# Performance work log

Measured on AMD Instinct MI355X. Metric: run time of the kernel, lower is better.

The kernel has to match this reference:

```python
import jax, jax.numpy as jnp
import numpy as np

B, S = 32, 256          # sequences, tokens per sequence (prefill)
DIM, NH, NKV, HD = 2048, 16, 16, 128
CLS, GRID, BASE = 1, 16, 10000


def precompute_freqs_cis_2d(grid_size, n_elem, base, cls_token_num):
    half = n_elem // 2
    freqs = 1.0 / (base ** (np.arange(0, half, 2)[: half // 2].astype(np.float32) / half))
    t = np.arange(grid_size, dtype=np.float32)
    fr = np.outer(t, freqs)                      # [grid, half//2]
    fg = np.concatenate([
        np.broadcast_to(fr[:, None, :], (grid_size, grid_size, fr.shape[1])),
        np.broadcast_to(fr[None, :, :], (grid_size, grid_size, fr.shape[1])),
    ], axis=-1)                                  # [grid, grid, half]
    cache = np.stack([np.cos(fg), np.sin(fg)], axis=-1).reshape(grid_size * grid_size, half, 2)
    cond = np.concatenate([np.zeros((cls_token_num, half, 2), np.float32), cache.astype(np.float32)], axis=0)
    return jnp.asarray(cond)                     # [cls+grid^2, half, 2]

FREQS = precompute_freqs_cis_2d(GRID, HD, BASE, CLS)


def _apply_rope(x, fc):
    # x: [T, H, HD], fc: [T, HD//2, 2]
    xr = x.reshape(x.shape[0], x.shape[1], HD // 2, 2)
    c = fc[:, None, :, 0]
    s = fc[:, None, :, 1]
    out = jnp.stack([xr[..., 0] * c - xr[..., 1] * s,
                     xr[..., 1] * c + xr[..., 0] * s], axis=-1)
    return out.reshape(x.shape)


def setup_inputs() -> dict:
    key = jax.random.key(0)
    k1, k2, k3 = jax.random.split(key, 3)
    x = jax.random.normal(k1, (B * S, DIM), dtype=jnp.float32)
    positions = jnp.tile(jnp.arange(S, dtype=jnp.int32), B)  # per-seq positions 0..S-1
    total_kv = (NH + 2 * NKV) * HD
    wqkv = jax.random.normal(k2, (total_kv, DIM), dtype=jnp.float32) * 0.02
    wo = jax.random.normal(k3, (DIM, DIM), dtype=jnp.float32) * 0.02
    return {"x": x, "positions": positions, "wqkv": wqkv, "wo": wo}


def reference(x, positions, wqkv, wo):
    T = x.shape[0]
    kv_size = NKV * HD
    qkv = x @ wqkv.T                               # [T, dim + 2*kv_size]
    xq, xk, xv = jnp.split(qkv, [DIM, DIM + kv_size], axis=-1)
    q = xq.reshape(T, NH, HD)
    k = xk.reshape(T, NKV, HD)
    v = xv.reshape(T, NKV, HD)

    fc = FREQS[positions]                          # [T, HD//2, 2]
    q = _apply_rope(q, fc)
    k = _apply_rope(k, fc)

    # paged attention (prefill): causal attention within each sequence
    qb = q.reshape(B, S, NH, HD)
    kb = k.reshape(B, S, NKV, HD)
    vb = v.reshape(B, S, NKV, HD)
    scale = HD ** -0.5
    scores = jnp.einsum("bqhd,bkhd->bhqk", qb, kb) * scale   # [B,H,S,S]
    causal = jnp.tril(jnp.ones((S, S), dtype=bool))
    scores = jnp.where(causal[None, None], scores, jnp.finfo(scores.dtype).min)
    attn = jax.nn.softmax(scores, axis=-1)
    out = jnp.einsum("bhqk,bkhd->bqhd", attn, vb).reshape(T, DIM)
    return out @ wo.T
```

## Files before the change

### kernel.cpp

```cpp
#include <hip/hip_runtime.h>
#include <cstddef>


typedef float    f32x4 __attribute__((ext_vector_type(4)));
typedef _Float16 f16x8 __attribute__((ext_vector_type(8)));
typedef _Float16 f16x4 __attribute__((ext_vector_type(4)));

#define LOG2E 1.4426950408889634f
#define NLOG2B_32 (-0.41524101186192697f)

__device__ static inline f32x4 mfma16x32(f16x8 a, f16x8 b, f32x4 c) {
  return __builtin_amdgcn_mfma_f32_16x16x32_f16(a, b, c, 0, 0, 0);
}

__device__ static inline void gload16(const void* g, void* lds) {
  __builtin_amdgcn_global_load_lds(
      (const __attribute__((address_space(1))) unsigned int*)g,
      (__attribute__((address_space(3))) unsigned int*)lds, 16, 0, 0);
}

#define BAR()    asm volatile("s_barrier" ::: "memory")
#define VMCNT6() asm volatile("s_waitcnt vmcnt(6)" ::: "memory")

__global__ void cvt3_f32_f16(const float* __restrict__ s0, _Float16* __restrict__ d0,
                             const float* __restrict__ s1, _Float16* __restrict__ d1,
                             const float* __restrict__ s2, _Float16* __restrict__ d2) {
  int i = blockIdx.x * blockDim.x + threadIdx.x;
  const float* src; _Float16* dst;
  if (i < 4194304)      { src = s0; dst = d0; }
  else if (i < 7340032) { src = s1; dst = d1; i -= 4194304; }
  else                  { src = s2; dst = d2; i -= 7340032; }
  f32x4 v = *(const f32x4*)(src + (size_t)i * 4);
  f16x4 o;
  o[0] = (_Float16)v[0]; o[1] = (_Float16)v[1];
  o[2] = (_Float16)v[2]; o[3] = (_Float16)v[3];
  *(f16x4*)(dst + (size_t)i * 4) = o;
}

template <typename OutT>
__global__ void __launch_bounds__(512, 2)
gemm_bt5(const _Float16* __restrict__ A, const _Float16* __restrict__ Bt,
         OutT* __restrict__ C, int M, int N, int K) {
  __shared__ __attribute__((aligned(16))) _Float16 Ab[2][256 * 64];
  __shared__ __attribute__((aligned(16))) _Float16 Bb[2][256 * 64];

  const int tid  = threadIdx.x;
  const int lane = tid & 63;
  const int w    = tid >> 6;
  const int wm   = w >> 2, wn = w & 3;
  const int g    = lane >> 4, li = lane & 15;

  const int nwg = (int)gridDim.x;
  const int cpx = nwg >> 3;
  const int bid = (int)blockIdx.x;
  const int swz = (bid & 7) * cpx + (bid >> 3);
  const int nbn = N >> 8;
  const int bm  = (swz / nbn) << 8;
  const int bn  = (swz % nbn) << 8;
  const int NT  = K >> 6;

  const int srow = tid >> 3;
  const int scol = ((tid & 7) ^ (srow & 7)) * 8;
  const _Float16* gA = A  + (size_t)(bm + srow) * K + scol;
  const _Float16* gB = Bt + (size_t)(bn + srow) * K + scol;
  const int sdst = w * 1024;

  auto stage = [&](const _Float16* gbase, _Float16* lbase, int h, int kt) {
    const _Float16* gp = gbase + (size_t)h * 128 * K + kt;
    char* lp = (char*)lbase + h * 16384;
#pragma unroll
    for (int j = 0; j < 2; ++j)
      gload16(gp + (size_t)j * 64 * K, lp + j * 8192 + sdst);
  };

  auto rdfrag = [&](const _Float16* buf, int row, int k2) -> f16x8 {
    const int pc = ((k2 << 2) + g) ^ (li & 7);
    return *(const f16x8*)((const char*)buf + row * 128 + pc * 16);
  };

  f32x4 acc[8][4] = {};

  stage(gA, Ab[0], 0, 0);
  stage(gB, Bb[0], 0, 0);
  stage(gB, Bb[0], 1, 0);
  stage(gA, Ab[0], 1, 0);
  stage(gA, Ab[1], 0, (NT > 1) ? 64 : 0);
  VMCNT6();
  BAR();

  for (int T = 0; T < NT; ++T) {
    const int cb = T & 1, nb = cb ^ 1;
    const _Float16* Ac = Ab[cb];
    const _Float16* Bc = Bb[cb];
    const int ktN  = (T + 1 < NT) ? (T + 1) << 6 : 0;
    const int ktN2 = (T + 2 < NT) ? (T + 2) << 6 : 0;

    f16x8 af0[4][2], af1[4][2], bf0[2][2], bf1[2][2];

#pragma unroll
    for (int m = 0; m < 4; ++m)
#pragma unroll
      for (int k2 = 0; k2 < 2; ++k2)
        af0[m][k2] = rdfrag(Ac, wm * 128 + m * 16 + li, k2);
#pragma unroll
    for (int n = 0; n < 2; ++n)
#pragma unroll
      for (int k2 = 0; k2 < 2; ++k2)
        bf0[n][k2] = rdfrag(Bc, wn * 64 + n * 16 + li, k2);
    stage(gB, Bb[nb], 0, ktN);
    __builtin_amdgcn_s_setprio(1);
#pragma unroll
    for (int m = 0; m < 4; ++m)
#pragma unroll
      for (int n = 0; n < 2; ++n)
#pragma unroll
        for (int k2 = 0; k2 < 2; ++k2)
          acc[m][n] = mfma16x32(af0[m][k2], bf0[n][k2], acc[m][n]);
    __builtin_amdgcn_s_setprio(0);
    VMCNT6();
    BAR();

#pragma unroll
    for (int n = 0; n < 2; ++n)
#pragma unroll
      for (int k2 = 0; k2 < 2; ++k2)
        bf1[n][k2] = rdfrag(Bc, wn * 64 + (n + 2) * 16 + li, k2);
    stage(gB, Bb[nb], 1, ktN);
    __builtin_amdgcn_s_setprio(1);
#pragma unroll
    for (int m = 0; m < 4; ++m)
#pragma unroll
      for (int n = 0; n < 2; ++n)
#pragma unroll
        for (int k2 = 0; k2 < 2; ++k2)
          acc[m][n + 2] = mfma16x32(af0[m][k2], bf1[n][k2], acc[m][n + 2]);
    __builtin_amdgcn_s_setprio(0);
    VMCNT6();
    BAR();

#pragma unroll
    for (int m = 0; m < 4; ++m)
#pragma unroll
      for (int k2 = 0; k2 < 2; ++k2)
        af1[m][k2] = rdfrag(Ac, wm * 128 + (m + 4) * 16 + li, k2);
    stage(gA, Ab[nb], 1, ktN);
    __builtin_amdgcn_s_setprio(1);
#pragma unroll
    for (int m = 0; m < 4; ++m)
#pragma unroll
      for (int n = 0; n < 2; ++n)
#pragma unroll
        for (int k2 = 0; k2 < 2; ++k2)
          acc[m + 4][n] = mfma16x32(af1[m][k2], bf0[n][k2], acc[m + 4][n]);
    __builtin_amdgcn_s_setprio(0);
    VMCNT6();
    BAR();

    stage(gA, Ab[cb], 0, ktN2);
    __builtin_amdgcn_s_setprio(1);
#pragma unroll
    for (int m = 0; m < 4; ++m)
#pragma unroll
      for (int n = 0; n < 2; ++n)
#pragma unroll
        for (int k2 = 0; k2 < 2; ++k2)
          acc[m + 4][n + 2] = mfma16x32(af1[m][k2], bf1[n][k2], acc[m + 4][n + 2]);
    __builtin_amdgcn_s_setprio(0);
    VMCNT6();
    BAR();
  }

  asm volatile("s_waitcnt vmcnt(0)" ::: "memory");

#pragma unroll
  for (int m = 0; m < 8; ++m)
#pragma unroll
    for (int n = 0; n < 4; ++n)
#pragma unroll
      for (int r = 0; r < 4; ++r) {
        const int row = bm + wm * 128 + m * 16 + g * 4 + r;
        const int col = bn + wn * 64 + n * 16 + li;
        C[(size_t)row * N + col] = (OutT)acc[m][n][r];
      }
}

__global__ void rope_kernel(_Float16* __restrict__ qkv,
                            const int* __restrict__ positions) {
  const int idx = blockIdx.x * blockDim.x + threadIdx.x;
  const int ch = idx & 15;
  const int hh = (idx >> 4) & 31;
  const int t  = idx >> 9;
  _Float16* p = qkv + (size_t)t * 6144 + hh * 128 + ch * 8;
  const int pos = positions[t];
  f16x8 v = *(const f16x8*)p;
  f16x8 o;
  if (pos == 0) {
#pragma unroll
    for (int u = 0; u < 8; ++u) o[u] = (_Float16)0.f;
  } else {
    const int gi = pos - 1;
    const float tv = (ch < 8) ? (float)(gi >> 4) : (float)(gi & 15);
#pragma unroll
    for (int u = 0; u < 4; ++u) {
      const int k2 = (ch * 4 + u) & 31;
      const float freq = exp2f((float)k2 * NLOG2B_32);
      const float ang = tv * freq;
      float s, c;
      sincosf(ang, &s, &c);
      const float x0 = (float)v[2 * u];
      const float x1 = (float)v[2 * u + 1];
      o[2 * u]     = (_Float16)(x0 * c - x1 * s);
      o[2 * u + 1] = (_Float16)(x1 * c + x0 * s);
    }
  }
  *(f16x8*)p = o;
}

__global__ void __launch_bounds__(512)
attn_kernel(const _Float16* __restrict__ qkv, _Float16* __restrict__ O) {
  const int b  = blockIdx.x >> 4;
  const int h  = blockIdx.x & 15;
  const int tb = b << 8;
  const int tid = threadIdx.x;
  const int lane = tid & 63;
  const int w = tid >> 6;
  const int g = lane >> 4, li = lane & 15;

  __shared__ __attribute__((aligned(16))) _Float16 Ks[64 * 128];
  __shared__ __attribute__((aligned(16))) _Float16 Vt[128 * 64];
  __shared__ __attribute__((aligned(16))) _Float16 Ps[8][32 * 40];

  const int qb[2]   = {w, 15 - w};
  const int qrow[2] = {qb[0] * 16, qb[1] * 16};
  const int kmax[2] = {qb[0] >> 2, qb[1] >> 2};

  f16x8 qf[2][4];
#pragma unroll
  for (int rb = 0; rb < 2; ++rb)
#pragma unroll
    for (int ks = 0; ks < 4; ++ks)
      qf[rb][ks] = *(const f16x8*)(qkv + (size_t)(tb + qrow[rb] + li) * 6144
                                   + h * 128 + ks * 32 + g * 8);

  f32x4 oacc[2][8] = {};
  float m_r[2][4], l_r[2][4];
#pragma unroll
  for (int rb = 0; rb < 2; ++rb)
#pragma unroll
    for (int r = 0; r < 4; ++r) { m_r[rb][r] = -1e30f; l_r[rb][r] = 0.f; }

  const float scale = 0.08838834764831845f;

  for (int kt = 0; kt < 4; ++kt) {
#pragma unroll
    for (int i = 0; i < 2; ++i) {
      const int s = i * 512 + tid;
      const int key = s >> 4;
      const int sch = (s & 15) ^ (key & 7);
      const _Float16* gk = qkv + (size_t)(tb + kt * 64 + key) * 6144
                           + 2048 + h * 128 + sch * 8;
      gload16(gk, (char*)Ks + (i * 512 + (tid & ~63)) * 16);
    }
#pragma unroll
    for (int i = 0; i < 2; ++i) {
      const int s = i * 512 + tid;
      const int key = s >> 4;
      const int chv = s & 15;
      f16x8 v = *(const f16x8*)(qkv + (size_t)(tb + kt * 64 + key) * 6144
                                + 4096 + h * 128 + chv * 8);
#pragma unroll
      for (int e = 0; e < 8; ++e) {
        const int d = chv * 8 + e;
        const int blk = ((key >> 3) ^ (d & 7) ^ ((d >> 3) & 7)) & 7;
        Vt[d * 64 + blk * 8 + (key & 7)] = v[e];
      }
    }
    __syncthreads();

    const bool act[2] = {kt <= kmax[0], kt <= kmax[1]};
    if (act[0] || act[1]) {
      f32x4 sacc[2][4] = {};
#pragma unroll
      for (int ks = 0; ks < 4; ++ks) {
        f16x8 kf[4];
#pragma unroll
        for (int cb = 0; cb < 4; ++cb) {
          const int key = cb * 16 + li;
          const int chunk = (ks * 4 + g) ^ (key & 7);
          kf[cb] = *(const f16x8*)((const char*)Ks + key * 256 + chunk * 16);
        }
#pragma unroll
        for (int rb = 0; rb < 2; ++rb)
          if (act[rb])
#pragma unroll
            for (int cb = 0; cb < 4; ++cb)
              sacc[rb][cb] = mfma16x32(qf[rb][ks], kf[cb], sacc[rb][cb]);
      }
#pragma unroll
      for (int rb = 0; rb < 2; ++rb) {
        if (!act[rb]) continue;
#pragma unroll
        for (int r = 0; r < 4; ++r) {
          const int q = qrow[rb] + g * 4 + r;
          float mx = -1e30f;
#pragma unroll
          for (int cb = 0; cb < 4; ++cb) {
            float sv = sacc[rb][cb][r] * scale;
            const int key = kt * 64 + cb * 16 + li;
            sv = (key <= q) ? sv : -1e30f;
            sacc[rb][cb][r] = sv;
            mx = fmaxf(mx, sv);
          }
#pragma unroll
          for (int off = 1; off < 16; off <<= 1)
            mx = fmaxf(mx, __shfl_xor(mx, off));
          const float mold = m_r[rb][r];
          const float mnew = fmaxf(mold, mx);
          const float alpha = exp2f((mold - mnew) * LOG2E);
          float rsum = 0.f;
#pragma unroll
          for (int cb = 0; cb < 4; ++cb) {
            const float pv = exp2f((sacc[rb][cb][r] - mnew) * LOG2E);
            sacc[rb][cb][r] = pv;
            rsum += pv;
          }
#pragma unroll
          for (int off = 1; off < 16; off <<= 1)
            rsum += __shfl_xor(rsum, off);
          m_r[rb][r] = mnew;
          l_r[rb][r] = l_r[rb][r] * alpha + rsum;
#pragma unroll
          for (int db = 0; db < 8; ++db)
            oacc[rb][db][r] *= alpha;
        }
      }
#pragma unroll
      for (int ks2 = 0; ks2 < 2; ++ks2) {
#pragma unroll
        for (int rb = 0; rb < 2; ++rb) {
          if (!act[rb]) continue;
#pragma unroll
          for (int cbh = 0; cbh < 2; ++cbh) {
            const int cb = ks2 * 2 + cbh;
#pragma unroll
            for (int r = 0; r < 4; ++r)
              Ps[w][(rb * 16 + g * 4 + r) * 40 + cbh * 16 + li] =
                  (_Float16)sacc[rb][cb][r];
          }
        }
        asm volatile("s_waitcnt lgkmcnt(0)" ::: "memory");
        f16x8 pa[2];
#pragma unroll
        for (int rb = 0; rb < 2; ++rb)
          if (act[rb])
            pa[rb] = *(const f16x8*)(&Ps[w][(rb * 16 + li) * 40 + g * 8]);
#pragma unroll
        for (int db = 0; db < 8; ++db) {
          const int d = db * 16 + li;
          const int keych = ks2 * 4 + g;
          const int blk = (keych ^ (d & 7) ^ ((d >> 3) & 7)) & 7;
          const f16x8 vf = *(const f16x8*)(&Vt[d * 64 + blk * 8]);
#pragma unroll
          for (int rb = 0; rb < 2; ++rb)
            if (act[rb])
              oacc[rb][db] = mfma16x32(pa[rb], vf, oacc[rb][db]);
        }
      }
    }
    __syncthreads();
  }
#pragma unroll
  for (int rb = 0; rb < 2; ++rb)
#pragma unroll
    for (int db = 0; db < 8; ++db)
#pragma unroll
      for (int r = 0; r < 4; ++r) {
        const int row = tb + qrow[rb] + g * 4 + r;
        const int col = h * 128 + db * 16 + li;
        O[(size_t)row * 2048 + col] = (_Float16)(oacc[rb][db][r] / l_r[rb][r]);
      }
}

extern "C" void kernel_launch(void* const* d_in, const int* in_sizes, int n_in,
                              void* d_out, int out_size, void* d_ws, size_t ws_size,
                              hipStream_t stream) {
  const float* x         = (const float*)d_in[0];
  const int*   positions = (const int*)d_in[1];
  const float* wqkv      = (const float*)d_in[2];
  const float* wo        = (const float*)d_in[3];
  float* out = (float*)d_out;

  char* ws = (char*)d_ws;
  _Float16* qkv    = (_Float16*)(ws);
  _Float16* xf     = (_Float16*)(ws + 100663296);
  _Float16* wqkvf  = (_Float16*)(ws + 134217728);
  _Float16* wof    = (_Float16*)(ws + 159383552);
  _Float16* of     = xf;

  cvt3_f32_f16<<<32768, 256, 0, stream>>>(x, xf, wqkv, wqkvf, wo, wof);

  gemm_bt5<_Float16><<<768, 512, 0, stream>>>(xf, wqkvf, qkv, 8192, 6144, 2048);

  rope_kernel<<<16384, 256, 0, stream>>>(qkv, positions);

  attn_kernel<<<512, 512, 0, stream>>>(qkv, of);

  gemm_bt5<float><<<256, 512, 0, stream>>>(of, wof, out, 8192, 2048, 2048);
}
```

Before: 367.8 us.

## Fuse RoPE into attention and restructure GEMM staging into K-halves

```diff
diff --git a/kernel.cpp b/kernel.cpp
--- a/kernel.cpp
+++ b/kernel.cpp
@@ -20,7 +20,7 @@
 }
 
 #define BAR()    asm volatile("s_barrier" ::: "memory")
-#define VMCNT6() asm volatile("s_waitcnt vmcnt(6)" ::: "memory")
+#define VMCNT4() asm volatile("s_waitcnt vmcnt(4)" ::: "memory")
 
 __global__ void cvt3_f32_f16(const float* __restrict__ s0, _Float16* __restrict__ d0,
                              const float* __restrict__ s1, _Float16* __restrict__ d1,
@@ -39,7 +39,7 @@
 
 template <typename OutT>
 __global__ void __launch_bounds__(512, 2)
-gemm_bt5(const _Float16* __restrict__ A, const _Float16* __restrict__ Bt,
+gemm_bt7(const _Float16* __restrict__ A, const _Float16* __restrict__ Bt,
          OutT* __restrict__ C, int M, int N, int K) {
   __shared__ __attribute__((aligned(16))) _Float16 Ab[2][256 * 64];
   __shared__ __attribute__((aligned(16))) _Float16 Bb[2][256 * 64];
@@ -59,114 +59,100 @@
   const int bn  = (swz % nbn) << 8;
   const int NT  = K >> 6;
 
-  const int srow = tid >> 3;
-  const int scol = ((tid & 7) ^ (srow & 7)) * 8;
+  const int srow = tid >> 2;
+  const int scol = ((tid & 3) ^ ((tid >> 3) & 3)) * 8;
   const _Float16* gA = A  + (size_t)(bm + srow) * K + scol;
   const _Float16* gB = Bt + (size_t)(bn + srow) * K + scol;
   const int sdst = w * 1024;
 
-  auto stage = [&](const _Float16* gbase, _Float16* lbase, int h, int kt) {
-    const _Float16* gp = gbase + (size_t)h * 128 * K + kt;
-    char* lp = (char*)lbase + h * 16384;
+  auto stage = [&](const _Float16* gbase, _Float16* lbase, int kh, int kt) {
+    const _Float16* gp = gbase + kh * 32 + kt;
+    char* lp = (char*)lbase + kh * 16384;
 #pragma unroll
     for (int j = 0; j < 2; ++j)
-      gload16(gp + (size_t)j * 64 * K, lp + j * 8192 + sdst);
+      gload16(gp + (size_t)j * 128 * K, lp + j * 8192 + sdst);
   };
 
-  auto rdfrag = [&](const _Float16* buf, int row, int k2) -> f16x8 {
-    const int pc = ((k2 << 2) + g) ^ (li & 7);
-    return *(const f16x8*)((const char*)buf + row * 128 + pc * 16);
+  auto rdfrag = [&](const _Float16* buf, int row, int kh) -> f16x8 {
+    const int pc = g ^ ((row >> 1) & 3);
+    return *(const f16x8*)((const char*)buf + kh * 16384 + row * 64 + pc * 16);
   };
 
   f32x4 acc[8][4] = {};
 
   stage(gA, Ab[0], 0, 0);
   stage(gB, Bb[0], 0, 0);
+  stage(gA, Ab[0], 1, 0);
   stage(gB, Bb[0], 1, 0);
-  stage(gA, Ab[0], 1, 0);
-  stage(gA, Ab[1], 0, (NT > 1) ? 64 : 0);
-  VMCNT6();
+  asm volatile("s_waitcnt vmcnt(0)" ::: "memory");
   BAR();
 
   for (int T = 0; T < NT; ++T) {
     const int cb = T & 1, nb = cb ^ 1;
     const _Float16* Ac = Ab[cb];
     const _Float16* Bc = Bb[cb];
-    const int ktN  = (T + 1 < NT) ? (T + 1) << 6 : 0;
-    const int ktN2 = (T + 2 < NT) ? (T + 2) << 6 : 0;
-
-    f16x8 af0[4][2], af1[4][2], bf0[2][2], bf1[2][2];
-
-#pragma unroll
-    for (int m = 0; m < 4; ++m)
-#pragma unroll
-      for (int k2 = 0; k2 < 2; ++k2)
-        af0[m][k2] = rdfrag(Ac, wm * 128 + m * 16 + li, k2);
+    const int ktN = (T + 1 < NT) ? (T + 1) << 6 : 0;
+
+    f16x8 af[8], bf[2], bf2[2];
+
+#pragma unroll
+    for (int m = 0; m < 8; ++m)
+      af[m] = rdfrag(Ac, wm * 128 + m * 16 + li, 0);
 #pragma unroll
     for (int n = 0; n < 2; ++n)
-#pragma unroll
-      for (int k2 = 0; k2 < 2; ++k2)
-        bf0[n][k2] = rdfrag(Bc, wn * 64 + n * 16 + li, k2);
+      bf[n] = rdfrag(Bc, wn * 64 + n * 16 + li, 0);
+    stage(gA, Ab[nb], 0, ktN);
+    __builtin_amdgcn_s_setprio(1);
+#pragma unroll
+    for (int m = 0; m < 8; ++m)
+#pragma unroll
+      for (int n = 0; n < 2; ++n)
+        acc[m][n] = mfma16x32(af[m], bf[n], acc[m][n]);
+    __builtin_amdgcn_s_setprio(0);
+    BAR();
+
+#pragma unroll
+    for (int n = 0; n < 2; ++n)
+      bf2[n] = rdfrag(Bc, wn * 64 + (n + 2) * 16 + li, 0);
     stage(gB, Bb[nb], 0, ktN);
     __builtin_amdgcn_s_setprio(1);
 #pragma unroll
-    for (int m = 0; m < 4; ++m)
+    for (int m = 0; m < 8; ++m)
 #pragma unroll
       for (int n = 0; n < 2; ++n)
-#pragma unroll
-        for (int k2 = 0; k2 < 2; ++k2)
-          acc[m][n] = mfma16x32(af0[m][k2], bf0[n][k2], acc[m][n]);
+        acc[m][n + 2] = mfma16x32(af[m], bf2[n], acc[m][n + 2]);
     __builtin_amdgcn_s_setprio(0);
-    VMCNT6();
+    VMCNT4();
     BAR();
 
 #pragma unroll
+    for (int m = 0; m < 8; ++m)
+      af[m] = rdfrag(Ac, wm * 128 + m * 16 + li, 1);
+#pragma unroll
     for (int n = 0; n < 2; ++n)
-#pragma unroll
-      for (int k2 = 0; k2 < 2; ++k2)
-        bf1[n][k2] = rdfrag(Bc, wn * 64 + (n + 2) * 16 + li, k2);
+      bf[n] = rdfrag(Bc, wn * 64 + n * 16 + li, 1);
+    stage(gA, Ab[nb], 1, ktN);
+    __builtin_amdgcn_s_setprio(1);
+#pragma unroll
+    for (int m = 0; m < 8; ++m)
+#pragma unroll
+      for (int n = 0; n < 2; ++n)
+        acc[m][n] = mfma16x32(af[m], bf[n], acc[m][n]);
+    __builtin_amdgcn_s_setprio(0);
+    BAR();
+
+#pragma unroll
+    for (int n = 0; n < 2; ++n)
+      bf2[n] = rdfrag(Bc, wn * 64 + (n + 2) * 16 + li, 1);
     stage(gB, Bb[nb], 1, ktN);
     __builtin_amdgcn_s_setprio(1);
 #pragma unroll
-    for (int m = 0; m < 4; ++m)
+    for (int m = 0; m < 8; ++m)
 #pragma unroll
       for (int n = 0; n < 2; ++n)
-#pragma unroll
-        for (int k2 = 0; k2 < 2; ++k2)
-          acc[m][n + 2] = mfma16x32(af0[m][k2], bf1[n][k2], acc[m][n + 2]);
+        acc[m][n + 2] = mfma16x32(af[m], bf2[n], acc[m][n + 2]);
     __builtin_amdgcn_s_setprio(0);
-    VMCNT6();
-    BAR();
-
-#pragma unroll
-    for (int m = 0; m < 4; ++m)
-#pragma unroll
-      for (int k2 = 0; k2 < 2; ++k2)
-        af1[m][k2] = rdfrag(Ac, wm * 128 + (m + 4) * 16 + li, k2);
-    stage(gA, Ab[nb], 1, ktN);
-    __builtin_amdgcn_s_setprio(1);
-#pragma unroll
-    for (int m = 0; m < 4; ++m)
-#pragma unroll
-      for (int n = 0; n < 2; ++n)
-#pragma unroll
-        for (int k2 = 0; k2 < 2; ++k2)
-          acc[m + 4][n] = mfma16x32(af1[m][k2], bf0[n][k2], acc[m + 4][n]);
-    __builtin_amdgcn_s_setprio(0);
-    VMCNT6();
-    BAR();
-
-    stage(gA, Ab[cb], 0, ktN2);
-    __builtin_amdgcn_s_setprio(1);
-#pragma unroll
-    for (int m = 0; m < 4; ++m)
-#pragma unroll
-      for (int n = 0; n < 2; ++n)
-#pragma unroll
-        for (int k2 = 0; k2 < 2; ++k2)
-          acc[m + 4][n + 2] = mfma16x32(af1[m][k2], bf1[n][k2], acc[m + 4][n + 2]);
-    __builtin_amdgcn_s_setprio(0);
-    VMCNT6();
+    VMCNT4();
     BAR();
   }
 
@@ -184,40 +170,9 @@
       }
 }
 
-__global__ void rope_kernel(_Float16* __restrict__ qkv,
-                            const int* __restrict__ positions) {
-  const int idx = blockIdx.x * blockDim.x + threadIdx.x;
-  const int ch = idx & 15;
-  const int hh = (idx >> 4) & 31;
-  const int t  = idx >> 9;
-  _Float16* p = qkv + (size_t)t * 6144 + hh * 128 + ch * 8;
-  const int pos = positions[t];
-  f16x8 v = *(const f16x8*)p;
-  f16x8 o;
-  if (pos == 0) {
-#pragma unroll
-    for (int u = 0; u < 8; ++u) o[u] = (_Float16)0.f;
-  } else {
-    const int gi = pos - 1;
-    const float tv = (ch < 8) ? (float)(gi >> 4) : (float)(gi & 15);
-#pragma unroll
-    for (int u = 0; u < 4; ++u) {
-      const int k2 = (ch * 4 + u) & 31;
-      const float freq = exp2f((float)k2 * NLOG2B_32);
-      const float ang = tv * freq;
-      float s, c;
-      sincosf(ang, &s, &c);
-      const float x0 = (float)v[2 * u];
-      const float x1 = (float)v[2 * u + 1];
-      o[2 * u]     = (_Float16)(x0 * c - x1 * s);
-      o[2 * u + 1] = (_Float16)(x1 * c + x0 * s);
-    }
-  }
-  *(f16x8*)p = o;
-}
-
 __global__ void __launch_bounds__(512)
-attn_kernel(const _Float16* __restrict__ qkv, _Float16* __restrict__ O) {
+attn_kernel(const _Float16* __restrict__ qkv, _Float16* __restrict__ O,
+            const int* __restrict__ positions) {
   const int b  = blockIdx.x >> 4;
   const int h  = blockIdx.x & 15;
   const int tb = b << 8;
@@ -229,6 +184,17 @@
   __shared__ __attribute__((aligned(16))) _Float16 Ks[64 * 128];
   __shared__ __attribute__((aligned(16))) _Float16 Vt[128 * 64];
   __shared__ __attribute__((aligned(16))) _Float16 Ps[8][32 * 40];
+  __shared__ float2 tab[512];
+  __shared__ int    ptab[256];
+
+  {
+    const float ang = (float)(tid >> 5) * exp2f((float)(tid & 31) * NLOG2B_32);
+    float s, c;
+    sincosf(ang, &s, &c);
+    tab[tid] = make_float2(c, s);
+    if (tid < 256) ptab[tid] = positions[tb + tid];
+  }
+  __syncthreads();
 
   const int qb[2]   = {w, 15 - w};
   const int qrow[2] = {qb[0] * 16, qb[1] * 16};
@@ -236,11 +202,30 @@
 
   f16x8 qf[2][4];
 #pragma unroll
-  for (int rb = 0; rb < 2; ++rb)
-#pragma unroll
-    for (int ks = 0; ks < 4; ++ks)
-      qf[rb][ks] = *(const f16x8*)(qkv + (size_t)(tb + qrow[rb] + li) * 6144
-                                   + h * 128 + ks * 32 + g * 8);
+  for (int rb = 0; rb < 2; ++rb) {
+    const int pos = ptab[qrow[rb] + li];
+    const int iv = (pos - 1) >> 4, jv = (pos - 1) & 15;
+#pragma unroll
+    for (int ks = 0; ks < 4; ++ks) {
+      f16x8 v = *(const f16x8*)(qkv + (size_t)(tb + qrow[rb] + li) * 6144
+                                + h * 128 + ks * 32 + g * 8);
+      f16x8 o;
+      if (pos == 0) {
+#pragma unroll
+        for (int u = 0; u < 8; ++u) o[u] = (_Float16)0.f;
+      } else {
+        const int tv = (ks < 2) ? iv : jv;
+#pragma unroll
+        for (int u = 0; u < 4; ++u) {
+          const float2 cs = tab[tv * 32 + ((ks * 16 + g * 4 + u) & 31)];
+          const float x0 = (float)v[2 * u], x1 = (float)v[2 * u + 1];
+          o[2 * u]     = (_Float16)(x0 * cs.x - x1 * cs.y);
+          o[2 * u + 1] = (_Float16)(x1 * cs.x + x0 * cs.y);
+        }
+      }
+      qf[rb][ks] = o;
+    }
+  }
 
   f32x4 oacc[2][8] = {};
   float m_r[2][4], l_r[2][4];
@@ -256,10 +241,26 @@
     for (int i = 0; i < 2; ++i) {
       const int s = i * 512 + tid;
       const int key = s >> 4;
-      const int sch = (s & 15) ^ (key & 7);
-      const _Float16* gk = qkv + (size_t)(tb + kt * 64 + key) * 6144
-                           + 2048 + h * 128 + sch * 8;
-      gload16(gk, (char*)Ks + (i * 512 + (tid & ~63)) * 16);
+      const int c   = s & 15;
+      f16x8 v = *(const f16x8*)(qkv + (size_t)(tb + kt * 64 + key) * 6144
+                                + 2048 + h * 128 + c * 8);
+      const int pos = ptab[kt * 64 + key];
+      f16x8 o;
+      if (pos == 0) {
+#pragma unroll
+        for (int u = 0; u < 8; ++u) o[u] = (_Float16)0.f;
+      } else {
+        const int iv = (pos - 1) >> 4, jv = (pos - 1) & 15;
+        const int tv = (c < 8) ? iv : jv;
+#pragma unroll
+        for (int u = 0; u < 4; ++u) {
+          const float2 cs = tab[tv * 32 + ((c * 4 + u) & 31)];
+          const float x0 = (float)v[2 * u], x1 = (float)v[2 * u + 1];
+          o[2 * u]     = (_Float16)(x0 * cs.x - x1 * cs.y);
+          o[2 * u + 1] = (_Float16)(x1 * cs.x + x0 * cs.y);
+        }
+      }
+      *(f16x8*)((char*)Ks + key * 256 + (c ^ (key & 7)) * 16) = o;
     }
 #pragma unroll
     for (int i = 0; i < 2; ++i) {
@@ -399,11 +400,9 @@
 
   cvt3_f32_f16<<<32768, 256, 0, stream>>>(x, xf, wqkv, wqkvf, wo, wof);
 
-  gemm_bt5<_Float16><<<768, 512, 0, stream>>>(xf, wqkvf, qkv, 8192, 6144, 2048);
-
-  rope_kernel<<<16384, 256, 0, stream>>>(qkv, positions);
-
-  attn_kernel<<<512, 512, 0, stream>>>(qkv, of);
-
-  gemm_bt5<float><<<256, 512, 0, stream>>>(of, wof, out, 8192, 2048, 2048);
-}
+  gemm_bt7<_Float16><<<768, 512, 0, stream>>>(xf, wqkvf, qkv, 8192, 6144, 2048);
+
+  attn_kernel<<<512, 512, 0, stream>>>(qkv, of, positions);
+
+  gemm_bt7<float><<<256, 512, 0, stream>>>(of, wof, out, 8192, 2048, 2048);
+}
```

Measured after the change: 368.5 us. No clear change (+0.2%).
